# Kernel tuning notes

Hardware: AMD Instinct MI355X
Metric: run time of the kernel (lower is better)

Reference implementation:

```python
import jax, jax.numpy as jnp
import numpy as np
from jax.scipy.special import gammaln
from jax.scipy.linalg import solve_triangular

NUG_MULT = 4.0   # default tuneParm[0]
SMOOTH = 1.5     # default tuneParm[1] -> Matern nu=1.5


def setup_inputs() -> dict:
    key = jax.random.key(0)
    k1, k2, k3 = jax.random.split(key, 3)
    n, N, p, mMax = 128, 2048, 2, 64
    Y_data = jax.random.normal(k1, (n, N), dtype=jnp.float32)
    X_data = jax.random.normal(k2, (n, N, p), dtype=jnp.float32)
    NNmax = jax.random.randint(k3, (N, mMax), 0, N)
    # theta chosen so all exp/log transforms are well-behaved (see shape_source)
    theta = jnp.array([0.0, 0.5, -0.3, 0.0, 0.5, 0.0, 0.0, 0.0, 0.0, 0.0], dtype=jnp.float32)
    return {"Y_data": Y_data, "X_data": X_data, "theta": theta, "NNmax": NNmax, "m": 30}


def _neg_intlik(Y_data, X_data, theta, NNmax, m):
    n, N, p = X_data.shape
    inds = jnp.arange(N)
    scal = 1.0 / (jnp.arange(N, dtype=Y_data.dtype) + 1.0)
    logs = jnp.log(scal)

    # nug_fun / sigma_fun / scaling_x, vectorized over locations
    nugMean = jax.nn.relu(jnp.exp(logs * theta[1] + theta[0]) - 1e-5) + 1e-5   # (N,)
    nugSd = nugMean * NUG_MULT
    alpha = nugMean**2 / nugSd**2 + 2.0
    beta = nugMean * (alpha - 1.0)
    sigma = jnp.exp(logs * theta[4] + theta[3])                                 # (N,)
    scales_x = jnp.exp(logs[:, None] * theta[6 + p:6 + 2 * p][None, :]
                       + theta[6:6 + p][None, :])                               # (N,p)

    # variable neighbor count handled by zero-masking padded columns:
    # zeroed columns contribute 0 to the linear kernel and 0 to pairwise distances,
    # exactly matching the per-location ncol = min(i, m) truncation.
    NN = NNmax[:, :m]                                                           # (N,m)
    ncol = jnp.minimum(inds, m)
    colmask = (jnp.arange(m)[None, :] < ncol[:, None]).astype(Y_data.dtype)     # (N,m)
    s_col = jnp.sqrt(jnp.exp((jnp.arange(m, dtype=Y_data.dtype) + 1.0) * theta[2]))  # scaling_fun, (m,)

    Yg = jnp.transpose(Y_data[:, NN], (1, 0, 2))                                # (N,n,m)
    Ys = Yg * (s_col[None, None, :] * colmask[:, None, :])
    Xi = jnp.transpose(X_data, (1, 0, 2))                                       # (N,n,p)
    xz = jnp.all(Xi == 0, axis=(1, 2))                                          # per-call all-zero check
    Xs = jnp.where(xz[:, None, None], 0.0, Xi * scales_x[:, None, :])
    W = jnp.concatenate([Ys, Xs], axis=2)                                       # (N,n,m+p)

    lin = jnp.einsum('bik,bjk->bij', W, W)                                      # linear kernel

    lenScal = jnp.exp(theta[5]) * jnp.sqrt(2.0 * SMOOTH)
    Wd = W / lenScal
    sq = jnp.sum(Wd * Wd, axis=2)                                               # (N,n)
    r2 = sq[:, :, None] + sq[:, None, :] - 2.0 * jnp.einsum('bik,bjk->bij', Wd, Wd)
    r = jnp.sqrt(jnp.clip(r2, 0.0))
    c = jnp.sqrt(jnp.asarray(3.0, Y_data.dtype)) * r                            # Matern nu=1.5
    matern = (1.0 + c) * jnp.exp(-c)

    K = (lin + matern * (sigma**2)[:, None, None]) / nugMean[:, None, None]
    K = jnp.where((inds == 0)[:, None, None], 0.0, K)                           # i==0 -> G = I
    G = K + jnp.eye(n, dtype=K.dtype)[None, :, :]

    GChol = jnp.linalg.cholesky(G)                                              # (N,n,n)
    yT = solve_triangular(GChol, Y_data.T[:, :, None], lower=True)[..., 0]      # (N,n)

    alphaPost = alpha + n / 2.0
    betaPost = beta + 0.5 * jnp.sum(yT * yT, axis=1)
    logdet = jnp.sum(jnp.log(jnp.diagonal(GChol, axis1=-2, axis2=-1)), axis=1)
    loglik = (-logdet + alpha * jnp.log(beta) - alphaPost * jnp.log(betaPost)
              + gammaln(alphaPost) - gammaln(alpha))
    return -jnp.sum(loglik)


def reference(Y_data, X_data, theta, NNmax, m):
    # mode='intlik' of TransportMap.forward (scalar negative integrated loglik)
    return _neg_intlik(Y_data, X_data, theta, NNmax, m)
```

## Files before the change

kernel.cpp:

```cpp
#include <hip/hip_runtime.h>
#include <math.h>

#define N_COLS 2048
#define N_ROWS 128
#define KW     32
#define WST    36
#define PST    20

static __device__ __forceinline__ void factor_panel(
    const int p, const int l, float* __restrict__ P, float* __restrict__ yL,
    float* __restrict__ invd, float& ld, float& yb) {
  float pr0[16], pr1[16];
#pragma unroll
  for (int qd = 0; qd < 4; ++qd) {
    const float4 v0 = *(const float4*)&P[l * PST + 4 * qd];
    const float4 v1 = *(const float4*)&P[(l + 64) * PST + 4 * qd];
    pr0[4 * qd + 0] = v0.x; pr0[4 * qd + 1] = v0.y; pr0[4 * qd + 2] = v0.z; pr0[4 * qd + 3] = v0.w;
    pr1[4 * qd + 0] = v1.x; pr1[4 * qd + 1] = v1.y; pr1[4 * qd + 2] = v1.z; pr1[4 * qd + 3] = v1.w;
  }
  float py0 = yL[l], py1 = yL[l + 64];
  const int pbase = p << 4;
#pragma unroll
  for (int k = 0; k < 16; ++k) {
    const int prow = pbase + k;
    const int olane = prow & 63;
    const bool hi = prow >= 64;
    const float dk = __shfl(hi ? pr1[k] : pr0[k], olane, 64);
    const float yk = __shfl(hi ? py1 : py0, olane, 64);
    const float inv = __builtin_amdgcn_rcpf(dk);
    if (l == 0) { ld += 0.5f * __logf(dk); yb += yk * yk * inv; invd[k] = inv; }
    const float f0 = (l > prow) ? pr0[k] * inv : 0.0f;
    const float f1 = (l + 64 > prow) ? pr1[k] * inv : 0.0f;
#pragma unroll
    for (int j = k + 1; j < 16; ++j) {
      const float rk = __shfl(hi ? pr1[j] : pr0[j], olane, 64);
      pr0[j] = fmaf(-f0, rk, pr0[j]);
      pr1[j] = fmaf(-f1, rk, pr1[j]);
    }
    py0 = fmaf(-f0, yk, py0);
    py1 = fmaf(-f1, yk, py1);
  }
#pragma unroll
  for (int qd = 0; qd < 4; ++qd) {
    *(float4*)&P[l * PST + 4 * qd] =
        make_float4(pr0[4 * qd + 0], pr0[4 * qd + 1], pr0[4 * qd + 2], pr0[4 * qd + 3]);
    *(float4*)&P[(l + 64) * PST + 4 * qd] =
        make_float4(pr1[4 * qd + 0], pr1[4 * qd + 1], pr1[4 * qd + 2], pr1[4 * qd + 3]);
  }
  yL[l] = py0;
  yL[l + 64] = py1;
}

__global__ __launch_bounds__(512) void chol_main(
    const float* __restrict__ Y, const float* __restrict__ X,
    const float* __restrict__ theta, const int* __restrict__ NNmax,
    const int* __restrict__ mPtr, const int mMax, float* __restrict__ out) {
  __shared__ __align__(16) float uMem[5120];
  __shared__ float yL[N_ROWS];
  __shared__ float swL[N_ROWS];
  __shared__ __align__(16) float invd[16];
  __shared__ float smaskL[KW];
  __shared__ int nnL[KW];
  __shared__ int nzflag;
  float* const Wl = uMem;
  float* const P0 = uMem;
  float* const P1 = uMem + 2560;

  const int b = blockIdx.x;
  const int t = threadIdx.x;
  const int ti = t & 15;
  const int tj = t >> 4;

  const float th2 = theta[2];
  const float logs = -__logf((float)(b + 1));
  const float nug = fmaxf(__expf(theta[0] + theta[1] * logs) - 1e-5f, 0.0f) + 1e-5f;
  const float sigma = __expf(theta[3] + theta[4] * logs);
  const float sig2 = sigma * sigma;
  const float invNug = 1.0f / nug;
  const float invL2 = __expf(-2.0f * theta[5]) * (1.0f / 3.0f);
  const float sx0 = __expf(theta[6] + theta[8] * logs);
  const float sx1 = __expf(theta[7] + theta[9] * logs);
  int m = *mPtr; if (m > 30) m = 30;

  if (t == 0) nzflag = 0;
  if (t < KW) {
    nnL[t] = (t < m) ? NNmax[b * mMax + t] : 0;
    smaskL[t] = (t < m && t < b) ? __expf(0.5f * (float)(t + 1) * th2) : 0.0f;
  }
  __syncthreads();

  {
    const int i0 = t & 127;
    const int jb = t >> 7;
#pragma unroll
    for (int qq = 0; qq < 8; ++qq) {
      const int j = jb + 4 * qq;
      float v;
      if (j < m) {
        v = Y[i0 * N_COLS + nnL[j]] * smaskL[j];
      } else if (j < m + 2) {
        const int kc = j - m;
        v = X[(i0 * N_COLS + b) * 2 + kc] * ((kc == 0) ? sx0 : sx1);
      } else {
        v = 0.0f;
      }
      Wl[i0 * WST + j] = v;
    }
  }
  if (t < N_ROWS) {
    const float2 xv = ((const float2*)X)[t * N_COLS + b];
    if (xv.x != 0.0f || xv.y != 0.0f) atomicOr(&nzflag, 1);
    yL[t] = Y[t * N_COLS + b];
  }
  __syncthreads();
  if (nzflag == 0 && t < N_ROWS) {
    Wl[t * WST + m] = 0.0f;
    Wl[t * WST + m + 1] = 0.0f;
  }
  __syncthreads();

  float acc[8][4];
#pragma unroll
  for (int a = 0; a < 8; ++a)
#pragma unroll
    for (int c = 0; c < 4; ++c) acc[a][c] = 0.0f;

#pragma unroll 2
  for (int kk = 0; kk < KW; kk += 4) {
    float4 wc[4];
#pragma unroll
    for (int c = 0; c < 4; ++c)
      wc[c] = *(const float4*)&Wl[(tj + 32 * c) * WST + kk];
#pragma unroll
    for (int a = 0; a < 8; ++a) {
      const float4 wa = *(const float4*)&Wl[(ti + 16 * a) * WST + kk];
#pragma unroll
      for (int c = 0; c < 4; ++c) {
        float v = acc[a][c];
        v = fmaf(wa.x, wc[c].x, v);
        v = fmaf(wa.y, wc[c].y, v);
        v = fmaf(wa.z, wc[c].z, v);
        v = fmaf(wa.w, wc[c].w, v);
        acc[a][c] = v;
      }
    }
  }

  if (ti == (tj & 15)) {
    if (tj < 16) {
#pragma unroll
      for (int c = 0; c < 4; ++c) swL[tj + 32 * c] = acc[2 * c][c];
    } else {
#pragma unroll
      for (int c = 0; c < 4; ++c) swL[tj + 32 * c] = acc[2 * c + 1][c];
    }
  }
  __syncthreads();

  if (b != 0) {
    float swc[4];
#pragma unroll
    for (int c = 0; c < 4; ++c) swc[c] = swL[tj + 32 * c];
#pragma unroll 1
    for (int a = 0; a < 8; ++a) {
      const float swa = swL[ti + 16 * a];
#pragma unroll
      for (int c = 0; c < 4; ++c) {
        const float d = acc[a][c];
        float r2 = (swa + swc[c] - 2.0f * d) * invL2;
        r2 = fmaxf(r2, 0.0f);
        const float cc = sqrtf(3.0f * r2);
        const float mat = (1.0f + cc) * __expf(-cc);
        float g = fmaf(mat, sig2, d) * invNug;
        if (ti + 16 * a == tj + 32 * c) g += 1.0f;
        acc[a][c] = g;
      }
    }
  } else {
#pragma unroll
    for (int a = 0; a < 8; ++a)
#pragma unroll
      for (int c = 0; c < 4; ++c)
        acc[a][c] = (ti + 16 * a == tj + 32 * c) ? 1.0f : 0.0f;
  }

  if (tj < 16) {
#pragma unroll
    for (int a = 0; a < 8; ++a) P0[(ti + 16 * a) * PST + tj] = acc[a][0];
  }

  float ld = 0.0f, yb = 0.0f;
  for (int p = 0; p < 8; ++p) {
    float* const Pc = (p & 1) ? P1 : P0;
    float* const Pn = (p & 1) ? P0 : P1;
    __syncthreads();
    if (t < 64) {
#pragma unroll
      for (int a = 4; a < 8; ++a)
        *(float4*)&Pn[t * 40 + 4 * (a - 4)] =
            make_float4(acc[a][0], acc[a][1], acc[a][2], acc[a][3]);
      factor_panel(p, t, Pc, yL, invd, ld, yb);
#pragma unroll
      for (int a = 4; a < 8; ++a) {
        const float4 v = *(const float4*)&Pn[t * 40 + 4 * (a - 4)];
        acc[a][0] = v.x; acc[a][1] = v.y; acc[a][2] = v.z; acc[a][3] = v.w;
      }
    }
    __syncthreads();
    const int q = p + 1;
    if (q < 8) {
      const int b16q = 16 * q;
#pragma unroll 1
      for (int kk = 0; kk < 16; kk += 4) {
        const float4 iv4 = *(const float4*)&invd[kk];
        float4 rc4[4];
#pragma unroll
        for (int c = 0; c < 4; ++c)
          if (32 * c + 31 >= b16q)
            rc4[c] = *(const float4*)&Pc[(tj + 32 * c) * PST + kk];
#pragma unroll
        for (int a = 0; a < 8; ++a) {
          if (a >= q) {
            float4 ra = *(const float4*)&Pc[(ti + 16 * a) * PST + kk];
            ra.x *= iv4.x; ra.y *= iv4.y; ra.z *= iv4.z; ra.w *= iv4.w;
#pragma unroll
            for (int c = 0; c < 4; ++c) {
              if (32 * c + 31 >= b16q) {
                float v = acc[a][c];
                v = fmaf(-ra.x, rc4[c].x, v);
                v = fmaf(-ra.y, rc4[c].y, v);
                v = fmaf(-ra.z, rc4[c].z, v);
                v = fmaf(-ra.w, rc4[c].w, v);
                acc[a][c] = v;
              }
            }
          }
        }
      }
      if ((tj >> 4) == (q & 1)) {
        const int cq = q >> 1;
#pragma unroll
        for (int a = 0; a < 8; ++a) {
          if (a >= q) {
            const float v = (cq == 0) ? acc[a][0]
                          : (cq == 1) ? acc[a][1]
                          : (cq == 2) ? acc[a][2] : acc[a][3];
            Pn[(ti + 16 * a) * PST + (tj & 15)] = v;
          }
        }
      }
    }
  }

  if (t == 0) {
    const float alpha = 2.0625f;
    const float alphaPost = alpha + 64.0f;
    const float beta = 1.0625f * nug;
    const float betaPost = beta + 0.5f * yb;
    const float loglik = -ld + alpha * __logf(beta) - alphaPost * __logf(betaPost)
                       + lgammaf(alphaPost) - lgammaf(alpha);
    atomicAdd(out, -loglik);
  }
}

extern "C" void kernel_launch(void* const* d_in, const int* in_sizes, int n_in,
                              void* d_out, int out_size, void* d_ws, size_t ws_size,
                              hipStream_t stream) {
  const float* Y = (const float*)d_in[0];
  const float* X = (const float*)d_in[1];
  const float* theta = (const float*)d_in[2];
  const int* NNmax = (const int*)d_in[3];
  const int* mPtr = (const int*)d_in[4];
  float* out = (float*)d_out;
  const int mMax = in_sizes[3] / N_COLS;

  hipMemsetAsync(out, 0, sizeof(float) * out_size, stream);
  chol_main<<<N_COLS, 512, 0, stream>>>(Y, X, theta, NNmax, mPtr, mMax, out);
}
```

Before: 400.9 us.

## Double threads per block to 1024 with 4x4 register tiles per thread

Result: slower. 551.6 us (+37.6%).

```diff
diff --git a/kernel.cpp b/kernel.cpp
--- a/kernel.cpp
+++ b/kernel.cpp
@@ -51,7 +51,7 @@
   yL[l + 64] = py1;
 }
 
-__global__ __launch_bounds__(512) void chol_main(
+__global__ __launch_bounds__(1024) void chol_main(
     const float* __restrict__ Y, const float* __restrict__ X,
     const float* __restrict__ theta, const int* __restrict__ NNmax,
     const int* __restrict__ mPtr, const int mMax, float* __restrict__ out) {
@@ -68,33 +68,32 @@
 
   const int b = blockIdx.x;
   const int t = threadIdx.x;
-  const int ti = t & 15;
-  const int tj = t >> 4;
-
-  const float th2 = theta[2];
+  const int r = t & 31;
+  const int s = t >> 5;
+
   const float logs = -__logf((float)(b + 1));
   const float nug = fmaxf(__expf(theta[0] + theta[1] * logs) - 1e-5f, 0.0f) + 1e-5f;
   const float sigma = __expf(theta[3] + theta[4] * logs);
   const float sig2 = sigma * sigma;
   const float invNug = 1.0f / nug;
   const float invL2 = __expf(-2.0f * theta[5]) * (1.0f / 3.0f);
-  const float sx0 = __expf(theta[6] + theta[8] * logs);
-  const float sx1 = __expf(theta[7] + theta[9] * logs);
   int m = *mPtr; if (m > 30) m = 30;
 
   if (t == 0) nzflag = 0;
   if (t < KW) {
     nnL[t] = (t < m) ? NNmax[b * mMax + t] : 0;
-    smaskL[t] = (t < m && t < b) ? __expf(0.5f * (float)(t + 1) * th2) : 0.0f;
+    smaskL[t] = (t < m && t < b) ? __expf(0.5f * (float)(t + 1) * theta[2]) : 0.0f;
   }
   __syncthreads();
 
   {
     const int i0 = t & 127;
     const int jb = t >> 7;
-#pragma unroll
-    for (int qq = 0; qq < 8; ++qq) {
-      const int j = jb + 4 * qq;
+    const float sx0 = __expf(theta[6] + theta[8] * logs);
+    const float sx1 = __expf(theta[7] + theta[9] * logs);
+#pragma unroll
+    for (int qq = 0; qq < 4; ++qq) {
+      const int j = jb + 8 * qq;
       float v;
       if (j < m) {
         v = Y[i0 * N_COLS + nnL[j]] * smaskL[j];
@@ -119,21 +118,21 @@
   }
   __syncthreads();
 
-  float acc[8][4];
-#pragma unroll
-  for (int a = 0; a < 8; ++a)
+  float acc[4][4];
+#pragma unroll
+  for (int a = 0; a < 4; ++a)
 #pragma unroll
     for (int c = 0; c < 4; ++c) acc[a][c] = 0.0f;
 
-#pragma unroll 2
+#pragma unroll 1
   for (int kk = 0; kk < KW; kk += 4) {
     float4 wc[4];
 #pragma unroll
     for (int c = 0; c < 4; ++c)
-      wc[c] = *(const float4*)&Wl[(tj + 32 * c) * WST + kk];
-#pragma unroll
-    for (int a = 0; a < 8; ++a) {
-      const float4 wa = *(const float4*)&Wl[(ti + 16 * a) * WST + kk];
+      wc[c] = *(const float4*)&Wl[(s + 32 * c) * WST + kk];
+#pragma unroll
+    for (int a = 0; a < 4; ++a) {
+      const float4 wa = *(const float4*)&Wl[(r + 32 * a) * WST + kk];
 #pragma unroll
       for (int c = 0; c < 4; ++c) {
         float v = acc[a][c];
@@ -146,24 +145,19 @@
     }
   }
 
-  if (ti == (tj & 15)) {
-    if (tj < 16) {
-#pragma unroll
-      for (int c = 0; c < 4; ++c) swL[tj + 32 * c] = acc[2 * c][c];
-    } else {
-#pragma unroll
-      for (int c = 0; c < 4; ++c) swL[tj + 32 * c] = acc[2 * c + 1][c];
-    }
+  if (r == s) {
+#pragma unroll
+    for (int a = 0; a < 4; ++a) swL[r + 32 * a] = acc[a][a];
   }
   __syncthreads();
 
   if (b != 0) {
     float swc[4];
 #pragma unroll
-    for (int c = 0; c < 4; ++c) swc[c] = swL[tj + 32 * c];
+    for (int c = 0; c < 4; ++c) swc[c] = swL[s + 32 * c];
 #pragma unroll 1
-    for (int a = 0; a < 8; ++a) {
-      const float swa = swL[ti + 16 * a];
+    for (int a = 0; a < 4; ++a) {
+      const float swa = swL[r + 32 * a];
 #pragma unroll
       for (int c = 0; c < 4; ++c) {
         const float d = acc[a][c];
@@ -172,21 +166,21 @@
         const float cc = sqrtf(3.0f * r2);
         const float mat = (1.0f + cc) * __expf(-cc);
         float g = fmaf(mat, sig2, d) * invNug;
-        if (ti + 16 * a == tj + 32 * c) g += 1.0f;
+        if (r == s && a == c) g += 1.0f;
         acc[a][c] = g;
       }
     }
   } else {
 #pragma unroll
-    for (int a = 0; a < 8; ++a)
+    for (int a = 0; a < 4; ++a)
 #pragma unroll
       for (int c = 0; c < 4; ++c)
-        acc[a][c] = (ti + 16 * a == tj + 32 * c) ? 1.0f : 0.0f;
-  }
-
-  if (tj < 16) {
-#pragma unroll
-    for (int a = 0; a < 8; ++a) P0[(ti + 16 * a) * PST + tj] = acc[a][0];
+        acc[a][c] = (r == s && a == c) ? 1.0f : 0.0f;
+  }
+
+  if (s < 16) {
+#pragma unroll
+    for (int a = 0; a < 4; ++a) P0[(r + 32 * a) * PST + s] = acc[a][0];
   }
 
   float ld = 0.0f, yb = 0.0f;
@@ -196,13 +190,13 @@
     __syncthreads();
     if (t < 64) {
 #pragma unroll
-      for (int a = 4; a < 8; ++a)
-        *(float4*)&Pn[t * 40 + 4 * (a - 4)] =
+      for (int a = 2; a < 4; ++a)
+        *(float4*)&Pn[t * 8 + 4 * (a - 2)] =
             make_float4(acc[a][0], acc[a][1], acc[a][2], acc[a][3]);
       factor_panel(p, t, Pc, yL, invd, ld, yb);
 #pragma unroll
-      for (int a = 4; a < 8; ++a) {
-        const float4 v = *(const float4*)&Pn[t * 40 + 4 * (a - 4)];
+      for (int a = 2; a < 4; ++a) {
+        const float4 v = *(const float4*)&Pn[t * 8 + 4 * (a - 2)];
         acc[a][0] = v.x; acc[a][1] = v.y; acc[a][2] = v.z; acc[a][3] = v.w;
       }
     }
@@ -217,11 +211,11 @@
 #pragma unroll
         for (int c = 0; c < 4; ++c)
           if (32 * c + 31 >= b16q)
-            rc4[c] = *(const float4*)&Pc[(tj + 32 * c) * PST + kk];
-#pragma unroll
-        for (int a = 0; a < 8; ++a) {
-          if (a >= q) {
-            float4 ra = *(const float4*)&Pc[(ti + 16 * a) * PST + kk];
+            rc4[c] = *(const float4*)&Pc[(s + 32 * c) * PST + kk];
+#pragma unroll
+        for (int a = 0; a < 4; ++a) {
+          if (32 * a + 31 >= b16q) {
+            float4 ra = *(const float4*)&Pc[(r + 32 * a) * PST + kk];
             ra.x *= iv4.x; ra.y *= iv4.y; ra.z *= iv4.z; ra.w *= iv4.w;
 #pragma unroll
             for (int c = 0; c < 4; ++c) {
@@ -237,15 +231,15 @@
           }
         }
       }
-      if ((tj >> 4) == (q & 1)) {
+      if ((s >> 4) == (q & 1)) {
         const int cq = q >> 1;
 #pragma unroll
-        for (int a = 0; a < 8; ++a) {
-          if (a >= q) {
+        for (int a = 0; a < 4; ++a) {
+          if (32 * a + 31 >= b16q) {
             const float v = (cq == 0) ? acc[a][0]
                           : (cq == 1) ? acc[a][1]
                           : (cq == 2) ? acc[a][2] : acc[a][3];
-            Pn[(ti + 16 * a) * PST + (tj & 15)] = v;
+            Pn[(r + 32 * a) * PST + (s & 15)] = v;
           }
         }
       }
@@ -275,5 +269,5 @@
   const int mMax = in_sizes[3] / N_COLS;
 
   hipMemsetAsync(out, 0, sizeof(float) * out_size, stream);
-  chol_main<<<N_COLS, 512, 0, stream>>>(Y, X, theta, NNmax, mPtr, mMax, out);
+  chol_main<<<N_COLS, 1024, 0, stream>>>(Y, X, theta, NNmax, mPtr, mMax, out);
 }
```

## Halve block to 256 threads with 8x8 register tiles per thread

Applied to the files above, without the earlier changes.

New measurement: 445.5 us. +11.1%, slower.

```diff
diff --git a/kernel.cpp b/kernel.cpp
--- a/kernel.cpp
+++ b/kernel.cpp
@@ -51,7 +51,7 @@
   yL[l + 64] = py1;
 }
 
-__global__ __launch_bounds__(512) void chol_main(
+__global__ __launch_bounds__(256, 1) void chol_main(
     const float* __restrict__ Y, const float* __restrict__ X,
     const float* __restrict__ theta, const int* __restrict__ NNmax,
     const int* __restrict__ mPtr, const int mMax, float* __restrict__ out) {
@@ -71,30 +71,29 @@
   const int ti = t & 15;
   const int tj = t >> 4;
 
-  const float th2 = theta[2];
   const float logs = -__logf((float)(b + 1));
   const float nug = fmaxf(__expf(theta[0] + theta[1] * logs) - 1e-5f, 0.0f) + 1e-5f;
   const float sigma = __expf(theta[3] + theta[4] * logs);
   const float sig2 = sigma * sigma;
   const float invNug = 1.0f / nug;
   const float invL2 = __expf(-2.0f * theta[5]) * (1.0f / 3.0f);
-  const float sx0 = __expf(theta[6] + theta[8] * logs);
-  const float sx1 = __expf(theta[7] + theta[9] * logs);
   int m = *mPtr; if (m > 30) m = 30;
 
   if (t == 0) nzflag = 0;
   if (t < KW) {
     nnL[t] = (t < m) ? NNmax[b * mMax + t] : 0;
-    smaskL[t] = (t < m && t < b) ? __expf(0.5f * (float)(t + 1) * th2) : 0.0f;
+    smaskL[t] = (t < m && t < b) ? __expf(0.5f * (float)(t + 1) * theta[2]) : 0.0f;
   }
   __syncthreads();
 
   {
     const int i0 = t & 127;
     const int jb = t >> 7;
-#pragma unroll
-    for (int qq = 0; qq < 8; ++qq) {
-      const int j = jb + 4 * qq;
+    const float sx0 = __expf(theta[6] + theta[8] * logs);
+    const float sx1 = __expf(theta[7] + theta[9] * logs);
+#pragma unroll
+    for (int qq = 0; qq < 16; ++qq) {
+      const int j = jb + 2 * qq;
       float v;
       if (j < m) {
         v = Y[i0 * N_COLS + nnL[j]] * smaskL[j];
@@ -119,136 +118,125 @@
   }
   __syncthreads();
 
-  float acc[8][4];
+  float gr[8][8];
 #pragma unroll
   for (int a = 0; a < 8; ++a)
 #pragma unroll
-    for (int c = 0; c < 4; ++c) acc[a][c] = 0.0f;
-
+    for (int c = 0; c < 8; ++c) gr[a][c] = 0.0f;
+
+#pragma unroll
+  for (int g = 0; g < 2; ++g) {
 #pragma unroll 2
-  for (int kk = 0; kk < KW; kk += 4) {
-    float4 wc[4];
-#pragma unroll
-    for (int c = 0; c < 4; ++c)
-      wc[c] = *(const float4*)&Wl[(tj + 32 * c) * WST + kk];
-#pragma unroll
-    for (int a = 0; a < 8; ++a) {
-      const float4 wa = *(const float4*)&Wl[(ti + 16 * a) * WST + kk];
-#pragma unroll
-      for (int c = 0; c < 4; ++c) {
-        float v = acc[a][c];
-        v = fmaf(wa.x, wc[c].x, v);
-        v = fmaf(wa.y, wc[c].y, v);
-        v = fmaf(wa.z, wc[c].z, v);
-        v = fmaf(wa.w, wc[c].w, v);
-        acc[a][c] = v;
-      }
-    }
-  }
-
-  if (ti == (tj & 15)) {
-    if (tj < 16) {
-#pragma unroll
-      for (int c = 0; c < 4; ++c) swL[tj + 32 * c] = acc[2 * c][c];
-    } else {
-#pragma unroll
-      for (int c = 0; c < 4; ++c) swL[tj + 32 * c] = acc[2 * c + 1][c];
-    }
+    for (int kk = 0; kk < KW; kk += 4) {
+      float4 wc[4];
+#pragma unroll
+      for (int c = 0; c < 4; ++c)
+        wc[c] = *(const float4*)&Wl[(tj + 16 * (4 * g + c)) * WST + kk];
+#pragma unroll
+      for (int a = 0; a < 8; ++a) {
+        const float4 wa = *(const float4*)&Wl[(ti + 16 * a) * WST + kk];
+#pragma unroll
+        for (int c = 0; c < 4; ++c) {
+          float v = gr[a][4 * g + c];
+          v = fmaf(wa.x, wc[c].x, v);
+          v = fmaf(wa.y, wc[c].y, v);
+          v = fmaf(wa.z, wc[c].z, v);
+          v = fmaf(wa.w, wc[c].w, v);
+          gr[a][4 * g + c] = v;
+        }
+      }
+    }
+  }
+
+  if (ti == tj) {
+#pragma unroll
+    for (int a = 0; a < 8; ++a) swL[ti + 16 * a] = gr[a][a];
   }
   __syncthreads();
 
   if (b != 0) {
-    float swc[4];
-#pragma unroll
-    for (int c = 0; c < 4; ++c) swc[c] = swL[tj + 32 * c];
-#pragma unroll 1
+    float swc[8];
+#pragma unroll
+    for (int c = 0; c < 8; ++c) swc[c] = swL[tj + 16 * c];
+#pragma unroll 2
     for (int a = 0; a < 8; ++a) {
       const float swa = swL[ti + 16 * a];
 #pragma unroll
-      for (int c = 0; c < 4; ++c) {
-        const float d = acc[a][c];
+      for (int c = 0; c < 8; ++c) {
+        const float d = gr[a][c];
         float r2 = (swa + swc[c] - 2.0f * d) * invL2;
         r2 = fmaxf(r2, 0.0f);
         const float cc = sqrtf(3.0f * r2);
         const float mat = (1.0f + cc) * __expf(-cc);
         float g = fmaf(mat, sig2, d) * invNug;
-        if (ti + 16 * a == tj + 32 * c) g += 1.0f;
-        acc[a][c] = g;
+        if (ti + 16 * a == tj + 16 * c) g += 1.0f;
+        gr[a][c] = g;
       }
     }
   } else {
 #pragma unroll
     for (int a = 0; a < 8; ++a)
 #pragma unroll
-      for (int c = 0; c < 4; ++c)
-        acc[a][c] = (ti + 16 * a == tj + 32 * c) ? 1.0f : 0.0f;
-  }
-
-  if (tj < 16) {
-#pragma unroll
-    for (int a = 0; a < 8; ++a) P0[(ti + 16 * a) * PST + tj] = acc[a][0];
-  }
+      for (int c = 0; c < 8; ++c)
+        gr[a][c] = (ti + 16 * a == tj + 16 * c) ? 1.0f : 0.0f;
+  }
+
+#pragma unroll
+  for (int a = 0; a < 8; ++a) P0[(ti + 16 * a) * PST + tj] = gr[a][0];
 
   float ld = 0.0f, yb = 0.0f;
+#pragma unroll
   for (int p = 0; p < 8; ++p) {
     float* const Pc = (p & 1) ? P1 : P0;
     float* const Pn = (p & 1) ? P0 : P1;
     __syncthreads();
     if (t < 64) {
 #pragma unroll
-      for (int a = 4; a < 8; ++a)
-        *(float4*)&Pn[t * 40 + 4 * (a - 4)] =
-            make_float4(acc[a][0], acc[a][1], acc[a][2], acc[a][3]);
+      for (int a = 0; a < 8; ++a)
+        *(float4*)&Pn[t * 36 + 4 * a] = make_float4(gr[a][4], gr[a][5], gr[a][6], gr[a][7]);
       factor_panel(p, t, Pc, yL, invd, ld, yb);
 #pragma unroll
-      for (int a = 4; a < 8; ++a) {
-        const float4 v = *(const float4*)&Pn[t * 40 + 4 * (a - 4)];
-        acc[a][0] = v.x; acc[a][1] = v.y; acc[a][2] = v.z; acc[a][3] = v.w;
+      for (int a = 0; a < 8; ++a) {
+        const float4 v = *(const float4*)&Pn[t * 36 + 4 * a];
+        gr[a][4] = v.x; gr[a][5] = v.y; gr[a][6] = v.z; gr[a][7] = v.w;
       }
     }
     __syncthreads();
-    const int q = p + 1;
-    if (q < 8) {
-      const int b16q = 16 * q;
-#pragma unroll 1
-      for (int kk = 0; kk < 16; kk += 4) {
-        const float4 iv4 = *(const float4*)&invd[kk];
-        float4 rc4[4];
-#pragma unroll
-        for (int c = 0; c < 4; ++c)
-          if (32 * c + 31 >= b16q)
-            rc4[c] = *(const float4*)&Pc[(tj + 32 * c) * PST + kk];
-#pragma unroll
-        for (int a = 0; a < 8; ++a) {
-          if (a >= q) {
-            float4 ra = *(const float4*)&Pc[(ti + 16 * a) * PST + kk];
-            ra.x *= iv4.x; ra.y *= iv4.y; ra.z *= iv4.z; ra.w *= iv4.w;
-#pragma unroll
-            for (int c = 0; c < 4; ++c) {
-              if (32 * c + 31 >= b16q) {
-                float v = acc[a][c];
-                v = fmaf(-ra.x, rc4[c].x, v);
-                v = fmaf(-ra.y, rc4[c].y, v);
-                v = fmaf(-ra.z, rc4[c].z, v);
-                v = fmaf(-ra.w, rc4[c].w, v);
-                acc[a][c] = v;
+    if (p < 7) {
+      const int q = p + 1;
+#pragma unroll
+      for (int g = 0; g < 2; ++g) {
+        const int clo = (4 * g > q) ? 4 * g : q;
+        if (clo < 4 * g + 4) {
+#pragma unroll 2
+          for (int kk = 0; kk < 16; kk += 4) {
+            const float4 iv4 = *(const float4*)&invd[kk];
+            float4 rc4[4];
+#pragma unroll
+            for (int c = 0; c < 4; ++c)
+              if (4 * g + c >= clo)
+                rc4[c] = *(const float4*)&Pc[(tj + 16 * (4 * g + c)) * PST + kk];
+#pragma unroll
+            for (int a = q; a < 8; ++a) {
+              float4 ra = *(const float4*)&Pc[(ti + 16 * a) * PST + kk];
+              ra.x *= iv4.x; ra.y *= iv4.y; ra.z *= iv4.z; ra.w *= iv4.w;
+#pragma unroll
+              for (int c = 0; c < 4; ++c) {
+                if (4 * g + c >= clo) {
+                  float v = gr[a][4 * g + c];
+                  v = fmaf(-ra.x, rc4[c].x, v);
+                  v = fmaf(-ra.y, rc4[c].y, v);
+                  v = fmaf(-ra.z, rc4[c].z, v);
+                  v = fmaf(-ra.w, rc4[c].w, v);
+                  gr[a][4 * g + c] = v;
+                }
               }
             }
           }
         }
       }
-      if ((tj >> 4) == (q & 1)) {
-        const int cq = q >> 1;
-#pragma unroll
-        for (int a = 0; a < 8; ++a) {
-          if (a >= q) {
-            const float v = (cq == 0) ? acc[a][0]
-                          : (cq == 1) ? acc[a][1]
-                          : (cq == 2) ? acc[a][2] : acc[a][3];
-            Pn[(ti + 16 * a) * PST + (tj & 15)] = v;
-          }
-        }
-      }
+#pragma unroll
+      for (int a = q; a < 8; ++a) Pn[(ti + 16 * a) * PST + tj] = gr[a][q];
     }
   }
 
@@ -275,5 +263,5 @@
   const int mMax = in_sizes[3] / N_COLS;
 
   hipMemsetAsync(out, 0, sizeof(float) * out_size, stream);
-  chol_main<<<N_COLS, 512, 0, stream>>>(Y, X, theta, NNmax, mPtr, mMax, out);
+  chol_main<<<N_COLS, 256, 0, stream>>>(Y, X, theta, NNmax, mPtr, mMax, out);
 }
```
